# Performance work log

Measured on AMD Instinct MI355X. Metric: run time of the kernel, lower is better.

Reference implementation:

```python
import jax, jax.numpy as jnp
import numpy as np

EPS = 1e-5

def _layer_norm(x, w, b):
    mu = jnp.mean(x, axis=-1, keepdims=True)
    var = jnp.mean((x - mu) ** 2, axis=-1, keepdims=True)
    return (x - mu) * jax.lax.rsqrt(var + EPS) * w + b

def setup_inputs() -> dict:
    H = 2048
    B, T = 4, 2048
    key = jax.random.key(0)
    ks = jax.random.split(key, 12)
    s = 0.02
    return {
        "hidden_state": jax.random.normal(ks[0], (B, T, H), dtype=jnp.float32),
        "ln_w": jnp.ones((H,), jnp.float32),
        "ln_b": jnp.zeros((H,), jnp.float32),
        "Wk": jax.random.normal(ks[1], (H, H), jnp.float32) * s,
        "Wv": jax.random.normal(ks[2], (H, H), jnp.float32) * s,
        "Wr": jax.random.normal(ks[3], (H, H), jnp.float32) * s,
        "Wo": jax.random.normal(ks[4], (H, H), jnp.float32) * s,
        "mix_k": jax.random.uniform(ks[5], (H,), jnp.float32),
        "mix_v": jax.random.uniform(ks[6], (H,), jnp.float32),
        "mix_r": jax.random.uniform(ks[7], (H,), jnp.float32),
        "time_decay": jax.random.normal(ks[8], (H,), jnp.float32) * 0.5,
        "current_token_weight": jax.random.normal(ks[9], (H,), jnp.float32) * 0.5,
    }

def _wkv(k, v, time_decay, curr_w):
    # k, v: [B, T, H]; max-stabilized RWKV recurrence, scanned over time.
    B, T, H = k.shape
    decay = -jnp.exp(time_decay)  # [H]
    num0 = jnp.zeros((B, H), k.dtype)
    den0 = jnp.zeros((B, H), k.dtype)
    norm0 = jnp.full((B, H), -jnp.inf, k.dtype)

    def step(carry, kv):
        num, den, norm = carry
        kt, vt = kv  # [B, H]
        ct = curr_w + kt
        cn = jnp.maximum(ct, norm)
        e_prev = jnp.exp(norm - cn)
        e_cur = jnp.exp(ct - cn)
        out = (e_prev * num + e_cur * vt) / (e_prev * den + e_cur)
        dpn = decay + norm
        new_norm = jnp.maximum(dpn, kt)
        e_d = jnp.exp(dpn - new_norm)
        e_k = jnp.exp(kt - new_norm)
        return (e_d * num + e_k * vt, e_d * den + e_k, new_norm), out

    kT = jnp.swapaxes(k, 0, 1)  # [T, B, H]
    vT = jnp.swapaxes(v, 0, 1)
    (num, den, norm), outs = jax.lax.scan(step, (num0, den0, norm0), (kT, vT))
    return jnp.swapaxes(outs, 0, 1), num, den, norm

def reference(hidden_state, ln_w, ln_b, Wk, Wv, Wr, Wo, mix_k, mix_v, mix_r,
              time_decay, current_token_weight):
    residual = hidden_state
    x = _layer_norm(hidden_state, ln_w, ln_b)  # [B, T, H]
    B, T, H = x.shape
    # shifted input: previous token (zeros for t=0 since previous_state is None)
    sx = jnp.concatenate([jnp.zeros((B, 1, H), x.dtype), x[:, :-1, :]], axis=1)
    xk = sx + mix_k * (x - sx)
    xv = sx + mix_v * (x - sx)
    xr = sx + mix_r * (x - sx)
    r = jax.nn.sigmoid(jnp.einsum('bth,oh->bto', xr, Wr))
    k = jnp.einsum('bth,oh->bto', xk, Wk)
    v = jnp.einsum('bth,oh->bto', xv, Wv)
    wkv, num, den, norm = _wkv(k, v, time_decay, current_token_weight)
    rwkv = jnp.einsum('bth,oh->bto', r * wkv, Wo)
    out = residual + rwkv
    return (out, (x[:, -1, :], num, den, norm))
```

## Files before the change

kernel.cpp:

```cpp
#include <hip/hip_runtime.h>
#include <hip/hip_bf16.h>
#include <stdint.h>

#define B_ 4
#define T_ 2048
#define H_ 2048
#define BT_ (B_ * T_)
#define BH_ (B_ * H_)
#define CH_ 32
#define CL_ (T_ / CH_)
#define NKT_ (H_ / 64)

typedef __bf16 bf16x8 __attribute__((ext_vector_type(8)));
typedef float f32x4 __attribute__((ext_vector_type(4)));

__device__ inline void async16(const void* g, void* l) {
  __builtin_amdgcn_global_load_lds(
      (__attribute__((address_space(1))) uint32_t*)(void*)(uintptr_t)g,
      (__attribute__((address_space(3))) uint32_t*)l,
      16, 0, 0);
}

__global__ __launch_bounds__(256) void cvt_bf16_kernel(
    const float* __restrict__ w0, const float* __restrict__ w1,
    const float* __restrict__ w2, const float* __restrict__ w3,
    __bf16* __restrict__ dst ) {
  const float* srcs[4] = {w0, w1, w2, w3};
  const float* src = srcs[blockIdx.y];
  __bf16* d = dst + (size_t)blockIdx.y * H_ * H_;
  int i = (blockIdx.x * 256 + threadIdx.x) * 8;
  const float4* s4 = (const float4*)(src + i);
  float4 a = s4[0], b = s4[1];
  bf16x8 o;
  o[0] = (__bf16)a.x; o[1] = (__bf16)a.y; o[2] = (__bf16)a.z; o[3] = (__bf16)a.w;
  o[4] = (__bf16)b.x; o[5] = (__bf16)b.y; o[6] = (__bf16)b.z; o[7] = (__bf16)b.w;
  *(bf16x8*)(d + i) = o;
}

__global__ __launch_bounds__(256) void ln_mix_kernel(
    const float* __restrict__ h, const float* __restrict__ lnw,
    const float* __restrict__ lnb, const float* __restrict__ mk,
    const float* __restrict__ mv, const float* __restrict__ mr,
    __bf16* __restrict__ xk, __bf16* __restrict__ xv, __bf16* __restrict__ xr,
    float* __restrict__ xlast) {
  const int row = blockIdx.x;
  const int t = row & (T_ - 1);
  const int tid = threadIdx.x;
  const bool hasprev = (t != 0);

  const float4* cr = (const float4*)(h + (size_t)row * H_);
  float4 c0 = cr[tid * 2 + 0], c1 = cr[tid * 2 + 1];
  float4 p0 = {0.f, 0.f, 0.f, 0.f}, p1 = {0.f, 0.f, 0.f, 0.f};
  if (hasprev) {
    const float4* pr = (const float4*)(h + (size_t)(row - 1) * H_);
    p0 = pr[tid * 2 + 0]; p1 = pr[tid * 2 + 1];
  }
  float4 red;
  red.x = c0.x + c0.y + c0.z + c0.w + c1.x + c1.y + c1.z + c1.w;
  red.y = c0.x * c0.x + c0.y * c0.y + c0.z * c0.z + c0.w * c0.w +
          c1.x * c1.x + c1.y * c1.y + c1.z * c1.z + c1.w * c1.w;
  red.z = p0.x + p0.y + p0.z + p0.w + p1.x + p1.y + p1.z + p1.w;
  red.w = p0.x * p0.x + p0.y * p0.y + p0.z * p0.z + p0.w * p0.w +
          p1.x * p1.x + p1.y * p1.y + p1.z * p1.z + p1.w * p1.w;
  #pragma unroll
  for (int off = 32; off; off >>= 1) {
    red.x += __shfl_down(red.x, off);
    red.y += __shfl_down(red.y, off);
    red.z += __shfl_down(red.z, off);
    red.w += __shfl_down(red.w, off);
  }
  __shared__ float4 rbuf[4];
  const int lane = tid & 63, wid = tid >> 6;
  if (lane == 0) rbuf[wid] = red;
  __syncthreads();
  float4 tot;
  tot.x = rbuf[0].x + rbuf[1].x + rbuf[2].x + rbuf[3].x;
  tot.y = rbuf[0].y + rbuf[1].y + rbuf[2].y + rbuf[3].y;
  tot.z = rbuf[0].z + rbuf[1].z + rbuf[2].z + rbuf[3].z;
  tot.w = rbuf[0].w + rbuf[1].w + rbuf[2].w + rbuf[3].w;

  const float inv = 1.0f / (float)H_;
  float mu = tot.x * inv;
  float rstd = rsqrtf(fmaxf(tot.y * inv - mu * mu, 0.f) + 1e-5f);
  float mup = tot.z * inv;
  float rstdp = rsqrtf(fmaxf(tot.w * inv - mup * mup, 0.f) + 1e-5f);

  float xc[8] = {c0.x, c0.y, c0.z, c0.w, c1.x, c1.y, c1.z, c1.w};
  float xp[8] = {p0.x, p0.y, p0.z, p0.w, p1.x, p1.y, p1.z, p1.w};
  const float4* W4 = (const float4*)lnw;
  const float4* Bv4 = (const float4*)lnb;
  const float4* MK4 = (const float4*)mk;
  const float4* MV4 = (const float4*)mv;
  const float4* MR4 = (const float4*)mr;
  float4 w0 = W4[tid * 2], w1 = W4[tid * 2 + 1];
  float4 b0 = Bv4[tid * 2], b1 = Bv4[tid * 2 + 1];
  float4 k0 = MK4[tid * 2], k1 = MK4[tid * 2 + 1];
  float4 v0 = MV4[tid * 2], v1 = MV4[tid * 2 + 1];
  float4 r0 = MR4[tid * 2], r1 = MR4[tid * 2 + 1];
  float wa[8] = {w0.x, w0.y, w0.z, w0.w, w1.x, w1.y, w1.z, w1.w};
  float ba[8] = {b0.x, b0.y, b0.z, b0.w, b1.x, b1.y, b1.z, b1.w};
  float ka[8] = {k0.x, k0.y, k0.z, k0.w, k1.x, k1.y, k1.z, k1.w};
  float va[8] = {v0.x, v0.y, v0.z, v0.w, v1.x, v1.y, v1.z, v1.w};
  float ra[8] = {r0.x, r0.y, r0.z, r0.w, r1.x, r1.y, r1.z, r1.w};

  bf16x8 ok_, ov_, or_;
  float xls[8];
  #pragma unroll
  for (int e = 0; e < 8; e++) {
    float x = (xc[e] - mu) * rstd * wa[e] + ba[e];
    float sx = hasprev ? (xp[e] - mup) * rstdp * wa[e] + ba[e] : 0.f;
    ok_[e] = (__bf16)(sx + ka[e] * (x - sx));
    ov_[e] = (__bf16)(sx + va[e] * (x - sx));
    or_[e] = (__bf16)(sx + ra[e] * (x - sx));
    xls[e] = x;
  }
  size_t obase = (size_t)row * H_ + tid * 8;
  *(bf16x8*)(xk + obase) = ok_;
  *(bf16x8*)(xv + obase) = ov_;
  *(bf16x8*)(xr + obase) = or_;
  if (t == T_ - 1) {
    float* dst = xlast + (size_t)(row >> 11) * H_ + tid * 8;
    #pragma unroll
    for (int e = 0; e < 8; e++) dst[e] = xls[e];
  }
}

template <int MODE>
__global__ __launch_bounds__(512, 1) void gemm_nt4(
    const __bf16* __restrict__ A, const __bf16* __restrict__ Bw,
    float* __restrict__ outf, __bf16* __restrict__ outb,
    const float* __restrict__ resid) {
  __shared__ __align__(16) char ring[2][65536];

  const int wgid = blockIdx.x;
  const int lin = (wgid & 7) * 32 + (wgid >> 3);
  const int bm = lin >> 3;
  const int bn = lin & 7;

  const int tid = threadIdx.x;
  const int lane = tid & 63, wv = tid >> 6;
  const int wm = wv >> 2;
  const int wn = wv & 3;
  const int rr = lane & 15, q = lane >> 4;

  f32x4 acc[8][4];
  #pragma unroll
  for (int m = 0; m < 8; m++)
    #pragma unroll
    for (int n = 0; n < 4; n++) acc[m][n] = (f32x4){0.f, 0.f, 0.f, 0.f};

  const char* Ag = (const char*)A + (size_t)(bm * 256) * (H_ * 2);
  const char* Bg = (const char*)Bw + (size_t)(bn * 256) * (H_ * 2);

  const int srow = wv * 8 + (lane >> 3);
  const int scol = ((lane & 7) ^ (lane >> 3)) << 4;

  const int rsw = rr & 7;

#define STAGE_TILE(kt_, buf_)                                                   \
  {                                                                             \
    char* base_ = ring[buf_];                                                   \
    _Pragma("unroll")                                                           \
    for (int mh_ = 0; mh_ < 2; mh_++) {                                         \
      const char* Mg_ = mh_ ? Bg : Ag;                                          \
      _Pragma("unroll")                                                         \
      for (int hh_ = 0; hh_ < 2; hh_++) {                                       \
        _Pragma("unroll")                                                       \
        for (int rd_ = 0; rd_ < 2; rd_++) {                                     \
          char* dst_ = base_ + mh_ * 32768 + hh_ * 16384 + rd_ * 8192 + wv * 1024; \
          const char* src_ = Mg_ + (size_t)(hh_ * 128 + rd_ * 64 + srow) * (H_ * 2) \
                             + (kt_) * 128 + scol;                              \
          async16(src_, dst_);                                                  \
        }                                                                       \
      }                                                                         \
    }                                                                           \
  }

  STAGE_TILE(0, 0);
  asm volatile("s_waitcnt vmcnt(0)" ::: "memory");
  __builtin_amdgcn_s_barrier();

  for (int kt = 0; kt < NKT_; kt++) {
    const int cur = kt & 1, nxt = cur ^ 1;
    const char* Alds = ring[cur];
    const char* Blds = ring[cur] + 32768;

    if (kt + 1 < NKT_) STAGE_TILE(kt + 1, nxt);

    bf16x8 bfr[4][2];
    #pragma unroll
    for (int ni = 0; ni < 4; ni++)
      #pragma unroll
      for (int ks = 0; ks < 2; ks++) {
        int row_t = wn * 64 + ni * 16 + rr;
        bfr[ni][ks] = *(const bf16x8*)(Blds + row_t * 128 +
                                       (((ks * 4 + q) ^ rsw) << 4));
      }

    #pragma unroll
    for (int p = 0; p < 4; p++) {
      bf16x8 af[2][2];
      #pragma unroll
      for (int mi = 0; mi < 2; mi++)
        #pragma unroll
        for (int ks = 0; ks < 2; ks++) {
          int row_t = wm * 128 + p * 32 + mi * 16 + rr;
          af[mi][ks] = *(const bf16x8*)(Alds + row_t * 128 +
                                        (((ks * 4 + q) ^ rsw) << 4));
        }
      #pragma unroll
      for (int ks = 0; ks < 2; ks++)
        #pragma unroll
        for (int mi = 0; mi < 2; mi++)
          #pragma unroll
          for (int ni = 0; ni < 4; ni++)
            acc[p * 2 + mi][ni] = __builtin_amdgcn_mfma_f32_16x16x32_bf16(
                af[mi][ks], bfr[ni][ks], acc[p * 2 + mi][ni], 0, 0, 0);
    }

    if (kt + 1 < NKT_) {
      asm volatile("s_waitcnt vmcnt(0)" ::: "memory");
      __builtin_amdgcn_s_barrier();
    }
  }
#undef STAGE_TILE

  const int r0 = bm * 256 + wm * 128 + q * 4;
  const int c0 = bn * 256 + wn * 64 + rr;
  #pragma unroll
  for (int m = 0; m < 8; m++) {
    #pragma unroll
    for (int n = 0; n < 4; n++) {
      int col = c0 + n * 16;
      #pragma unroll
      for (int rg = 0; rg < 4; rg++) {
        int rowg = r0 + m * 16 + rg;
        size_t idx = (size_t)rowg * H_ + col;
        float vv = acc[m][n][rg];
        if (MODE == 0) {
          outb[idx] = (__bf16)vv;
        } else if (MODE == 1) {
          outb[idx] = (__bf16)(1.f / (1.f + __expf(-vv)));
        } else {
          outf[idx] = resid[idx] + vv;
        }
      }
    }
  }
}

__global__ __launch_bounds__(256) void wkv_pass1(
    const __bf16* __restrict__ k, const __bf16* __restrict__ v,
    const float* __restrict__ td,
    float* __restrict__ cs_num, float* __restrict__ cs_den,
    float* __restrict__ cs_norm) {
  const int id = blockIdx.x * 256 + threadIdx.x;
  const int c = blockIdx.y;
  const int b = id >> 11;
  const int hh = id & (H_ - 1);
  const float decay = -__expf(td[hh]);
  float num = 0.f, den = 0.f, norm = -INFINITY;

  const int UN = 16;
  for (int t0 = c * CL_; t0 < (c + 1) * CL_; t0 += UN) {
    float kk[UN], vv[UN];
    size_t base = ((size_t)b * T_ + t0) * H_ + hh;
    #pragma unroll
    for (int i = 0; i < UN; i++) {
      kk[i] = (float)k[base + (size_t)i * H_];
      vv[i] = (float)v[base + (size_t)i * H_];
    }
    #pragma unroll
    for (int i = 0; i < UN; i++) {
      float dpn = decay + norm;
      float nn = fmaxf(dpn, kk[i]);
      float ed = __expf(dpn - nn), ek = __expf(kk[i] - nn);
      num = ed * num + ek * vv[i];
      den = ed * den + ek;
      norm = nn;
    }
  }
  cs_num[c * BH_ + id] = num;
  cs_den[c * BH_ + id] = den;
  cs_norm[c * BH_ + id] = norm;
}

__global__ __launch_bounds__(256) void wkv_scan(
    const float* __restrict__ cs_num, const float* __restrict__ cs_den,
    const float* __restrict__ cs_norm, const float* __restrict__ td,
    float* __restrict__ px_num, float* __restrict__ px_den,
    float* __restrict__ px_norm) {
  const int id = blockIdx.x * 256 + threadIdx.x;
  const int hh = id & (H_ - 1);
  const float Lw = -__expf(td[hh]) * (float)CL_;
  float num = 0.f, den = 0.f, norm = -INFINITY;
  for (int c = 0; c < CH_; c++) {
    px_num[c * BH_ + id] = num;
    px_den[c * BH_ + id] = den;
    px_norm[c * BH_ + id] = norm;
    float n_c = cs_num[c * BH_ + id];
    float d_c = cs_den[c * BH_ + id];
    float m_c = cs_norm[c * BH_ + id];
    float sn = norm + Lw;
    float on = fmaxf(sn, m_c);
    float ea = __expf(sn - on), eb = __expf(m_c - on);
    num = ea * num + eb * n_c;
    den = ea * den + eb * d_c;
    norm = on;
  }
}

__global__ __launch_bounds__(256) void wkv_pass2(
    const __bf16* __restrict__ k, const __bf16* __restrict__ v,
    const __bf16* __restrict__ r, const float* __restrict__ td,
    const float* __restrict__ cw,
    const float* __restrict__ px_num, const float* __restrict__ px_den,
    const float* __restrict__ px_norm,
    __bf16* __restrict__ a, float* __restrict__ ndn) {
  const int id = blockIdx.x * 256 + threadIdx.x;
  const int c = blockIdx.y;
  const int b = id >> 11;
  const int hh = id & (H_ - 1);
  const float decay = -__expf(td[hh]);
  const float cwv = cw[hh];
  float num = px_num[c * BH_ + id];
  float den = px_den[c * BH_ + id];
  float norm = px_norm[c * BH_ + id];

  const int UN = 16;
  for (int t0 = c * CL_; t0 < (c + 1) * CL_; t0 += UN) {
    float kk[UN], vv[UN], rrv[UN];
    size_t base = ((size_t)b * T_ + t0) * H_ + hh;
    #pragma unroll
    for (int i = 0; i < UN; i++) {
      kk[i] = (float)k[base + (size_t)i * H_];
      vv[i] = (float)v[base + (size_t)i * H_];
      rrv[i] = (float)r[base + (size_t)i * H_];
    }
    #pragma unroll
    for (int i = 0; i < UN; i++) {
      float kt = kk[i], vt = vv[i];
      float ct = cwv + kt;
      float cn = fmaxf(ct, norm);
      float ep = __expf(norm - cn), ec = __expf(ct - cn);
      float o = (ep * num + ec * vt) / (ep * den + ec);
      a[base + (size_t)i * H_] = (__bf16)(rrv[i] * o);
      float dpn = decay + norm;
      float nn = fmaxf(dpn, kt);
      float ed = __expf(dpn - nn), ek = __expf(kt - nn);
      num = ed * num + ek * vt;
      den = ed * den + ek;
      norm = nn;
    }
  }
  if (c == CH_ - 1) {
    ndn[id] = num;
    ndn[BH_ + id] = den;
    ndn[2 * BH_ + id] = norm;
  }
}

extern "C" void kernel_launch(void* const* d_in, const int* in_sizes, int n_in,
                              void* d_out, int out_size, void* d_ws, size_t ws_size,
                              hipStream_t stream) {
  const float* h   = (const float*)d_in[0];
  const float* lnw = (const float*)d_in[1];
  const float* lnb = (const float*)d_in[2];
  const float* Wk  = (const float*)d_in[3];
  const float* Wv  = (const float*)d_in[4];
  const float* Wr  = (const float*)d_in[5];
  const float* Wo  = (const float*)d_in[6];
  const float* mk  = (const float*)d_in[7];
  const float* mv  = (const float*)d_in[8];
  const float* mr  = (const float*)d_in[9];
  const float* td  = (const float*)d_in[10];
  const float* cw  = (const float*)d_in[11];

  char* ws = (char*)d_ws;
  const size_t MB = 1048576;
  __bf16* xk   = (__bf16*)(ws);
  __bf16* xv   = (__bf16*)(ws + 32 * MB);
  __bf16* xr   = (__bf16*)(ws + 64 * MB);
  __bf16* kbuf = (__bf16*)(ws + 96 * MB);
  __bf16* vbuf = (__bf16*)(ws + 128 * MB);
  __bf16* W16  = (__bf16*)(ws + 160 * MB);
  __bf16* Wk16 = W16;
  __bf16* Wv16 = Wk16 + (size_t)H_ * H_;
  __bf16* Wr16 = Wv16 + (size_t)H_ * H_;
  __bf16* Wo16 = Wr16 + (size_t)H_ * H_;
  float* cs_num  = (float*)(ws + 64 * MB);
  float* cs_den  = cs_num + (size_t)CH_ * BH_;
  float* cs_norm = cs_den + (size_t)CH_ * BH_;
  float* px_num  = cs_norm + (size_t)CH_ * BH_;
  float* px_den  = px_num + (size_t)CH_ * BH_;
  float* px_norm = px_den + (size_t)CH_ * BH_;

  float* out  = (float*)d_out;
  float* xlast = out + (size_t)BT_ * H_;
  float* ndn   = xlast + (size_t)B_ * H_;

  dim3 cg((H_ * H_) / (256 * 8), 4);
  cvt_bf16_kernel<<<cg, 256, 0, stream>>>(Wk, Wv, Wr, Wo, W16);

  ln_mix_kernel<<<BT_, 256, 0, stream>>>(h, lnw, lnb, mk, mv, mr, xk, xv, xr, xlast);

  const int gemm_blocks = (BT_ / 256) * (H_ / 256);
  gemm_nt4<0><<<gemm_blocks, 512, 0, stream>>>(xk, Wk16, nullptr, kbuf, nullptr);
  gemm_nt4<0><<<gemm_blocks, 512, 0, stream>>>(xv, Wv16, nullptr, vbuf, nullptr);
  gemm_nt4<1><<<gemm_blocks, 512, 0, stream>>>(xr, Wr16, nullptr, xv , nullptr);

  dim3 wg(BH_ / 256, CH_);
  wkv_pass1<<<wg, 256, 0, stream>>>(kbuf, vbuf, td, cs_num, cs_den, cs_norm);
  wkv_scan<<<BH_ / 256, 256, 0, stream>>>(cs_num, cs_den, cs_norm, td,
                                          px_num, px_den, px_norm);
  wkv_pass2<<<wg, 256, 0, stream>>>(kbuf, vbuf, xv, td, cw,
                                    px_num, px_den, px_norm,
                                    xk , ndn);

  gemm_nt4<2><<<gemm_blocks, 512, 0, stream>>>(xk, Wo16, out, nullptr, h);
}
```

Baseline: 362.9 us.

## Batch K/V/R projections into one launch with 128x128 tiles, two blocks per CU

The 256x256 single-block-per-CU GEMM is replaced by a 128x128-tile kernel with 256 threads and launch bounds that allow two resident blocks per CU. The K, V and R projections are merged into one 3072-block launch that picks the input, weight slice and output by tile index. The receptance output moves to its own workspace buffer. The aim is better latency hiding and load balance across CUs, at the cost of lower per-tile data reuse and more LDS traffic per MFMA.

```diff
diff --git a/kernel.cpp b/kernel.cpp
--- a/kernel.cpp
+++ b/kernel.cpp
@@ -69,15 +69,15 @@
     red.z += __shfl_down(red.z, off);
     red.w += __shfl_down(red.w, off);
   }
-  __shared__ float4 rbuf[4];
+  __shared__ float4 rbuf_[4];
   const int lane = tid & 63, wid = tid >> 6;
-  if (lane == 0) rbuf[wid] = red;
+  if (lane == 0) rbuf_[wid] = red;
   __syncthreads();
   float4 tot;
-  tot.x = rbuf[0].x + rbuf[1].x + rbuf[2].x + rbuf[3].x;
-  tot.y = rbuf[0].y + rbuf[1].y + rbuf[2].y + rbuf[3].y;
-  tot.z = rbuf[0].z + rbuf[1].z + rbuf[2].z + rbuf[3].z;
-  tot.w = rbuf[0].w + rbuf[1].w + rbuf[2].w + rbuf[3].w;
+  tot.x = rbuf_[0].x + rbuf_[1].x + rbuf_[2].x + rbuf_[3].x;
+  tot.y = rbuf_[0].y + rbuf_[1].y + rbuf_[2].y + rbuf_[3].y;
+  tot.z = rbuf_[0].z + rbuf_[1].z + rbuf_[2].z + rbuf_[3].z;
+  tot.w = rbuf_[0].w + rbuf_[1].w + rbuf_[2].w + rbuf_[3].w;
 
   const float inv = 1.0f / (float)H_;
   float mu = tot.x * inv;
@@ -125,36 +125,44 @@
   }
 }
 
-template <int MODE>
-__global__ __launch_bounds__(512, 1) void gemm_nt4(
-    const __bf16* __restrict__ A, const __bf16* __restrict__ Bw,
-    float* __restrict__ outf, __bf16* __restrict__ outb,
-    const float* __restrict__ resid) {
-  __shared__ __align__(16) char ring[2][65536];
-
+template <int WO>
+__global__ __launch_bounds__(256, 2) void gemm128(
+    const __bf16* __restrict__ A0, const __bf16* __restrict__ A1,
+    const __bf16* __restrict__ A2, const __bf16* __restrict__ Wb,
+    __bf16* __restrict__ o0, __bf16* __restrict__ o1, __bf16* __restrict__ o2,
+    float* __restrict__ outf, const float* __restrict__ resid) {
+  __shared__ __align__(16) char ring[2][32768];
+
+  const int NB = WO ? 1024 : 3072;
   const int wgid = blockIdx.x;
-  const int lin = (wgid & 7) * 32 + (wgid >> 3);
-  const int bm = lin >> 3;
-  const int bn = lin & 7;
+  const int lin = (wgid & 7) * (NB / 8) + (wgid >> 3);
+  int z, l;
+  if (WO) { z = 0; l = lin; }
+  else    { z = lin >> 10; l = lin & 1023; }
+  const int bm = l >> 4;
+  const int bn = l & 15;
+
+  const __bf16* A = (WO || z == 0) ? A0 : (z == 1 ? A1 : A2);
+  const __bf16* Bw = Wb + (size_t)z * H_ * H_;
+  __bf16* ob = (z == 0) ? o0 : (z == 1 ? o1 : o2);
 
   const int tid = threadIdx.x;
   const int lane = tid & 63, wv = tid >> 6;
-  const int wm = wv >> 2;
-  const int wn = wv & 3;
+  const int wm = wv >> 1;
+  const int wn = wv & 1;
   const int rr = lane & 15, q = lane >> 4;
 
-  f32x4 acc[8][4];
+  f32x4 acc[4][4];
   #pragma unroll
-  for (int m = 0; m < 8; m++)
+  for (int m = 0; m < 4; m++)
     #pragma unroll
     for (int n = 0; n < 4; n++) acc[m][n] = (f32x4){0.f, 0.f, 0.f, 0.f};
 
-  const char* Ag = (const char*)A + (size_t)(bm * 256) * (H_ * 2);
-  const char* Bg = (const char*)Bw + (size_t)(bn * 256) * (H_ * 2);
+  const char* Ag = (const char*)A + (size_t)(bm * 128) * (H_ * 2);
+  const char* Bg = (const char*)Bw + (size_t)(bn * 128) * (H_ * 2);
 
   const int srow = wv * 8 + (lane >> 3);
   const int scol = ((lane & 7) ^ (lane >> 3)) << 4;
-
   const int rsw = rr & 7;
 
 #define STAGE_TILE(kt_, buf_)                                                   \
@@ -164,14 +172,11 @@
     for (int mh_ = 0; mh_ < 2; mh_++) {                                         \
       const char* Mg_ = mh_ ? Bg : Ag;                                          \
       _Pragma("unroll")                                                         \
-      for (int hh_ = 0; hh_ < 2; hh_++) {                                       \
-        _Pragma("unroll")                                                       \
-        for (int rd_ = 0; rd_ < 2; rd_++) {                                     \
-          char* dst_ = base_ + mh_ * 32768 + hh_ * 16384 + rd_ * 8192 + wv * 1024; \
-          const char* src_ = Mg_ + (size_t)(hh_ * 128 + rd_ * 64 + srow) * (H_ * 2) \
-                             + (kt_) * 128 + scol;                              \
-          async16(src_, dst_);                                                  \
-        }                                                                       \
+      for (int rd_ = 0; rd_ < 4; rd_++) {                                       \
+        char* dst_ = base_ + mh_ * 16384 + rd_ * 4096 + wv * 1024;              \
+        const char* src_ = Mg_ + (size_t)(rd_ * 32 + srow) * (H_ * 2)           \
+                           + (kt_) * 128 + scol;                                \
+        async16(src_, dst_);                                                    \
       }                                                                         \
     }                                                                           \
   }
@@ -183,7 +188,7 @@
   for (int kt = 0; kt < NKT_; kt++) {
     const int cur = kt & 1, nxt = cur ^ 1;
     const char* Alds = ring[cur];
-    const char* Blds = ring[cur] + 32768;
+    const char* Blds = ring[cur] + 16384;
 
     if (kt + 1 < NKT_) STAGE_TILE(kt + 1, nxt);
 
@@ -198,24 +203,20 @@
       }
 
     #pragma unroll
-    for (int p = 0; p < 4; p++) {
-      bf16x8 af[2][2];
+    for (int mi = 0; mi < 4; mi++) {
+      bf16x8 af[2];
       #pragma unroll
-      for (int mi = 0; mi < 2; mi++)
-        #pragma unroll
-        for (int ks = 0; ks < 2; ks++) {
-          int row_t = wm * 128 + p * 32 + mi * 16 + rr;
-          af[mi][ks] = *(const bf16x8*)(Alds + row_t * 128 +
-                                        (((ks * 4 + q) ^ rsw) << 4));
-        }
+      for (int ks = 0; ks < 2; ks++) {
+        int row_t = wm * 64 + mi * 16 + rr;
+        af[ks] = *(const bf16x8*)(Alds + row_t * 128 +
+                                  (((ks * 4 + q) ^ rsw) << 4));
+      }
       #pragma unroll
       for (int ks = 0; ks < 2; ks++)
         #pragma unroll
-        for (int mi = 0; mi < 2; mi++)
-          #pragma unroll
-          for (int ni = 0; ni < 4; ni++)
-            acc[p * 2 + mi][ni] = __builtin_amdgcn_mfma_f32_16x16x32_bf16(
-                af[mi][ks], bfr[ni][ks], acc[p * 2 + mi][ni], 0, 0, 0);
+        for (int ni = 0; ni < 4; ni++)
+          acc[mi][ni] = __builtin_amdgcn_mfma_f32_16x16x32_bf16(
+              af[ks], bfr[ni][ks], acc[mi][ni], 0, 0, 0);
     }
 
     if (kt + 1 < NKT_) {
@@ -225,24 +226,24 @@
   }
 #undef STAGE_TILE
 
-  const int r0 = bm * 256 + wm * 128 + q * 4;
-  const int c0 = bn * 256 + wn * 64 + rr;
+  const int r0 = bm * 128 + wm * 64 + q * 4;
+  const int c0 = bn * 128 + wn * 64 + rr;
   #pragma unroll
-  for (int m = 0; m < 8; m++) {
-    #pragma unroll
-    for (int n = 0; n < 4; n++) {
-      int col = c0 + n * 16;
+  for (int mi = 0; mi < 4; mi++) {
+    #pragma unroll
+    for (int ni = 0; ni < 4; ni++) {
+      int col = c0 + ni * 16;
       #pragma unroll
       for (int rg = 0; rg < 4; rg++) {
-        int rowg = r0 + m * 16 + rg;
+        int rowg = r0 + mi * 16 + rg;
         size_t idx = (size_t)rowg * H_ + col;
-        float vv = acc[m][n][rg];
-        if (MODE == 0) {
-          outb[idx] = (__bf16)vv;
-        } else if (MODE == 1) {
-          outb[idx] = (__bf16)(1.f / (1.f + __expf(-vv)));
+        float vv = acc[mi][ni][rg];
+        if (WO) {
+          outf[idx] = resid[idx] + vv;
+        } else if (z == 2) {
+          ob[idx] = (__bf16)(1.f / (1.f + __expf(-vv)));
         } else {
-          outf[idx] = resid[idx] + vv;
+          ob[idx] = (__bf16)vv;
         }
       }
     }
@@ -384,10 +385,8 @@
   __bf16* kbuf = (__bf16*)(ws + 96 * MB);
   __bf16* vbuf = (__bf16*)(ws + 128 * MB);
   __bf16* W16  = (__bf16*)(ws + 160 * MB);
-  __bf16* Wk16 = W16;
-  __bf16* Wv16 = Wk16 + (size_t)H_ * H_;
-  __bf16* Wr16 = Wv16 + (size_t)H_ * H_;
-  __bf16* Wo16 = Wr16 + (size_t)H_ * H_;
+  __bf16* rbuf = (__bf16*)(ws + 192 * MB);
+  __bf16* Wo16 = W16 + 3 * (size_t)H_ * H_;
   float* cs_num  = (float*)(ws + 64 * MB);
   float* cs_den  = cs_num + (size_t)CH_ * BH_;
   float* cs_norm = cs_den + (size_t)CH_ * BH_;
@@ -404,18 +403,17 @@
 
   ln_mix_kernel<<<BT_, 256, 0, stream>>>(h, lnw, lnb, mk, mv, mr, xk, xv, xr, xlast);
 
-  const int gemm_blocks = (BT_ / 256) * (H_ / 256);
-  gemm_nt4<0><<<gemm_blocks, 512, 0, stream>>>(xk, Wk16, nullptr, kbuf, nullptr);
-  gemm_nt4<0><<<gemm_blocks, 512, 0, stream>>>(xv, Wv16, nullptr, vbuf, nullptr);
-  gemm_nt4<1><<<gemm_blocks, 512, 0, stream>>>(xr, Wr16, nullptr, xv , nullptr);
+  gemm128<0><<<3072, 256, 0, stream>>>(xk, xv, xr, W16, kbuf, vbuf, rbuf,
+                                       nullptr, nullptr);
 
   dim3 wg(BH_ / 256, CH_);
   wkv_pass1<<<wg, 256, 0, stream>>>(kbuf, vbuf, td, cs_num, cs_den, cs_norm);
   wkv_scan<<<BH_ / 256, 256, 0, stream>>>(cs_num, cs_den, cs_norm, td,
                                           px_num, px_den, px_norm);
-  wkv_pass2<<<wg, 256, 0, stream>>>(kbuf, vbuf, xv, td, cw,
+  wkv_pass2<<<wg, 256, 0, stream>>>(kbuf, vbuf, rbuf, td, cw,
                                     px_num, px_den, px_norm,
                                     xk , ndn);
 
-  gemm_nt4<2><<<gemm_blocks, 512, 0, stream>>>(xk, Wo16, out, nullptr, h);
-}
+  gemm128<1><<<1024, 256, 0, stream>>>(xk, nullptr, nullptr, Wo16,
+                                       nullptr, nullptr, nullptr, out, h);
+}
```

Measured after the change: 400.5 us. +10.3%, slower.
